# Performance work log

Hardware: AMD Instinct MI355X
Metric: run time of the kernel (lower is better)

The kernel has to match this reference:

```python
import jax, jax.numpy as jnp
import numpy as np

N_NODES = 50000
N_EDGES = 800000
IN_FEATS = 64
K = 4
OUT_FEATS = 256


def setup_inputs() -> dict:
    key = jax.random.key(0)
    k1, k2, k3, k4, k5 = jax.random.split(key, 5)
    signal = jax.random.normal(k1, (N_NODES, IN_FEATS), dtype=jnp.float32)
    src = jax.random.randint(k2, (N_EDGES,), 0, N_NODES, dtype=jnp.int32)
    dst = jax.random.randint(k3, (N_EDGES,), 0, N_NODES, dtype=jnp.int32)
    lambda_max = jnp.array([2.0], dtype=jnp.float32)  # normalized Laplacian bound
    W = jax.random.normal(k4, (IN_FEATS * K, OUT_FEATS), dtype=jnp.float32) * (1.0 / np.sqrt(IN_FEATS * K))
    b = jax.random.normal(k5, (OUT_FEATS,), dtype=jnp.float32) * 0.01
    return {"signal": signal, "src": src, "dst": dst, "lambda_max": lambda_max, "W": W, "b": b}


def reference(signal, src, dst, lambda_max, W, b):
    n = signal.shape[0]
    # in-degrees, clamped to >= 1, then D^{-1/2}
    deg = jax.ops.segment_sum(jnp.ones_like(dst, dtype=signal.dtype), dst, num_segments=n)
    d_sqrt = jnp.power(jnp.clip(deg, 1.0), -0.5)[:, None]  # [N,1]

    def unn_laplacian(x):
        # D^{-1/2} A D^{-1/2} x via gather-from-src, scatter-sum-to-dst
        h = (x * d_sqrt)[src]                                   # [E,f]
        agg = jax.ops.segment_sum(h, dst, num_segments=n)       # [N,f]
        return agg * d_sqrt

    X0 = signal
    Xs = [X0]
    if K > 1:
        re_norm = 2.0 / lambda_max  # broadcasts over nodes ([1] -> [N,f])
        X1 = -re_norm * unn_laplacian(X0) + X0 * (re_norm - 1.0)
        Xs.append(X1)
        for _ in range(2, K):
            Xi = -2.0 * re_norm * unn_laplacian(X1) + X1 * 2.0 * (re_norm - 1.0) - X0
            Xs.append(Xi)
            X1, X0 = Xi, X1
    Xt = jnp.concatenate(Xs, axis=1)  # [N, f*K]
    return jax.nn.relu(Xt @ W + b)
```

## Files before the change

kernel.cpp:

```cpp
#include <hip/hip_runtime.h>

#define NN 50000
#define NE 800000
#define F  64
#define OUTF 256
#define CAP 48
#define NT 3128

#define NPART 8
#define PART_NODES 6250
#define FILL_CHUNKS 256
#define CHUNK_E 3125

typedef __attribute__((ext_vector_type(8))) short    s16x8;
typedef __attribute__((ext_vector_type(8))) _Float16 f16x8;
typedef __attribute__((ext_vector_type(4))) float    f32x4;

static __device__ __forceinline__ unsigned short f2bf(float f) {
    unsigned u = __float_as_uint(f);
    u += 0x7fffu + ((u >> 16) & 1u);
    return (unsigned short)(u >> 16);
}
static __device__ __forceinline__ float bf2f(int h) {
    return __uint_as_float(((unsigned)(h & 0xffff)) << 16);
}
static __device__ __forceinline__ unsigned short f2h(float f) {
    _Float16 h = (_Float16)f;
    return __builtin_bit_cast(unsigned short, h);
}

__global__ __launch_bounds__(256) void fill_kernel(const int* __restrict__ src,
                                                   const int* __restrict__ dst,
                                                   int* __restrict__ cnt,
                                                   int* __restrict__ csr) {
    int part  = blockIdx.x & (NPART - 1);
    int chunk = blockIdx.x >> 3;
    int lo = part * PART_NODES;
    int e0 = chunk * CHUNK_E;
    int e1 = e0 + CHUNK_E;
    for (int e = e0 + threadIdx.x; e < e1; e += 256) {
        int d = dst[e];
        if ((unsigned)(d - lo) < (unsigned)PART_NODES) {
            int s = src[e];
            int k = atomicAdd(&cnt[d], 1);
            if (k < CAP) csr[d * CAP + k] = s;
        }
    }
}


__global__ __launch_bounds__(256) void prep_kernel(const float* __restrict__ sig,
                                                   const int* __restrict__ cnt,
                                                   const float* __restrict__ W,
                                                   unsigned short* __restrict__ XrowH,
                                                   unsigned short* __restrict__ XrowL,
                                                   unsigned short* __restrict__ XfF,
                                                   unsigned short* __restrict__ WfF) {
    int bid = blockIdx.x;
    if (bid < 3125) {
        int i = bid * 256 + threadIdx.x;
        int n = i >> 4, fq = i & 15;
        float d = rsqrtf(fmaxf((float)cnt[n], 1.0f));
        float4 v = *(const float4*)&sig[n * F + fq * 4];
        float yx = v.x * d, yy = v.y * d, yz = v.z * d, yw = v.w * d;
        unsigned short h0 = f2bf(yx), h1 = f2bf(yy), h2 = f2bf(yz), h3 = f2bf(yw);
        unsigned short l0 = f2bf(yx - bf2f(h0)), l1 = f2bf(yy - bf2f(h1));
        unsigned short l2 = f2bf(yz - bf2f(h2)), l3 = f2bf(yw - bf2f(h3));
        *(ushort4*)&XrowH[(size_t)n * 192 + fq * 4] = make_ushort4(h0, h1, h2, h3);
        *(ushort4*)&XrowL[(size_t)n * 192 + fq * 4] = make_ushort4(l0, l1, l2, l3);
        unsigned short u0 = f2h(v.x), u1 = f2h(v.y), u2 = f2h(v.z), u3 = f2h(v.w);
        int t = n >> 4, m = n & 15;
        int k0 = fq >> 3, qq = (fq >> 1) & 3, half = fq & 1;
        size_t base = ((size_t)((t * 8 + k0) * 64 + qq * 16 + m)) * 8 + half * 4;
        *(ushort4*)&XfF[base] = make_ushort4(u0, u1, u2, u3);
    } else {
        int id = (bid - 3125) * 256 + threadIdx.x;
        if (id < 8192) {
            int lane = id & 63, k0 = (id >> 6) & 7, ct = id >> 9;
            int n = lane & 15, q = lane >> 4;
            s16x8 h;
            #pragma unroll
            for (int j = 0; j < 8; ++j) {
                float x = W[(k0 * 32 + q * 8 + j) * OUTF + ct * 16 + n];
                h[j] = (short)f2h(x);
            }
            ((s16x8*)WfF)[id] = h;
        }
    }
}

__global__ __launch_bounds__(256) void lap_kernel(const int* __restrict__ cnt,
                                                  const int* __restrict__ csr,
                                                  const float* __restrict__ lm,
                                                  unsigned short* __restrict__ XrowH,
                                                  unsigned short* __restrict__ XrowL,
                                                  unsigned short* __restrict__ XfF, int p) {
    int lane = threadIdx.x & 63;
    int half = lane >> 5;
    int sub  = lane & 31;
    int q2   = sub >> 4;
    int fq   = sub & 15;
    int wid  = (blockIdx.x * blockDim.x + threadIdx.x) >> 6;
    int n    = wid * 2 + half;
    if (n >= NN) return;
    int dgf = cnt[n];
    int dg  = min(dgf, CAP);
    int cin = p - 1;
    int foff = fq << 2;

    float ax = 0.f, ay = 0.f, az = 0.f, aw = 0.f;
    for (int k = 0; k < dg; k += 16) {
        int   s[8];
        float w[8];
        ushort4 h[8];
        #pragma unroll
        for (int j = 0; j < 8; ++j) {
            int slot = k + q2 + 2 * j;
            int ok   = slot < dg;
            int si   = csr[n * CAP + slot];
            s[j] = ok ? si : 0;
            w[j] = ok ? 1.0f : 0.0f;
        }
        #pragma unroll
        for (int j = 0; j < 8; ++j)
            h[j] = *(const ushort4*)&XrowH[((size_t)s[j] * 3 + cin) * 64 + foff];
        #pragma unroll
        for (int j = 0; j < 8; ++j) {
            ax += bf2f(h[j].x) * w[j];
            ay += bf2f(h[j].y) * w[j];
            az += bf2f(h[j].z) * w[j];
            aw += bf2f(h[j].w) * w[j];
        }
    }
    ax += __shfl_xor(ax, 16);
    ay += __shfl_xor(ay, 16);
    az += __shfl_xor(az, 16);
    aw += __shfl_xor(aw, 16);

    float rn = 2.0f / lm[0];
    float dn = rsqrtf(fmaxf((float)dgf, 1.0f));
    float sq = sqrtf(fmaxf((float)dgf, 1.0f));
    ushort4 xh = *(const ushort4*)&XrowH[((size_t)n * 3 + cin) * 64 + foff];
    ushort4 xl = *(const ushort4*)&XrowL[((size_t)n * 3 + cin) * 64 + foff];
    float x1x = (bf2f(xh.x) + bf2f(xl.x)) * sq;
    float x1y = (bf2f(xh.y) + bf2f(xl.y)) * sq;
    float x1z = (bf2f(xh.z) + bf2f(xl.z)) * sq;
    float x1w = (bf2f(xh.w) + bf2f(xl.w)) * sq;
    float rx, ry, rz, rw;
    if (p == 1) {
        float c1 = rn - 1.0f;
        rx = -rn * dn * ax + x1x * c1;
        ry = -rn * dn * ay + x1y * c1;
        rz = -rn * dn * az + x1z * c1;
        rw = -rn * dn * aw + x1w * c1;
    } else {
        ushort4 zh = *(const ushort4*)&XrowH[((size_t)n * 3 + (p - 2)) * 64 + foff];
        ushort4 zl = *(const ushort4*)&XrowL[((size_t)n * 3 + (p - 2)) * 64 + foff];
        float c1 = 2.0f * (rn - 1.0f);
        rx = -2.0f * rn * dn * ax + x1x * c1 - (bf2f(zh.x) + bf2f(zl.x)) * sq;
        ry = -2.0f * rn * dn * ay + x1y * c1 - (bf2f(zh.y) + bf2f(zl.y)) * sq;
        rz = -2.0f * rn * dn * az + x1z * c1 - (bf2f(zh.z) + bf2f(zl.z)) * sq;
        rw = -2.0f * rn * dn * aw + x1w * c1 - (bf2f(zh.w) + bf2f(zl.w)) * sq;
    }

    float yx = rx * dn, yy = ry * dn, yz = rz * dn, yw = rw * dn;
    unsigned short yh0 = f2bf(yx), yh1 = f2bf(yy), yh2 = f2bf(yz), yh3 = f2bf(yw);
    if (q2 == 0) {
        if (p < 3)
            *(ushort4*)&XrowH[((size_t)n * 3 + p) * 64 + foff] = make_ushort4(yh0, yh1, yh2, yh3);
        unsigned short u0 = f2h(rx), u1 = f2h(ry), u2 = f2h(rz), u3 = f2h(rw);
        int t = n >> 4, m = n & 15;
        int k0 = p * 2 + (fq >> 3), qq = (fq >> 1) & 3, hf = fq & 1;
        size_t fbase = ((size_t)((t * 8 + k0) * 64 + qq * 16 + m)) * 8 + hf * 4;
        *(ushort4*)&XfF[fbase] = make_ushort4(u0, u1, u2, u3);
    } else if (p < 3) {
        unsigned short l0 = f2bf(yx - bf2f(yh0)), l1 = f2bf(yy - bf2f(yh1));
        unsigned short l2 = f2bf(yz - bf2f(yh2)), l3 = f2bf(yw - bf2f(yh3));
        *(ushort4*)&XrowL[((size_t)n * 3 + p) * 64 + foff] = make_ushort4(l0, l1, l2, l3);
    }
}

__global__ __launch_bounds__(512, 2) void gemm_kernel(const unsigned short* __restrict__ XfF,
                                                      const unsigned short* __restrict__ WfF,
                                                      const float* __restrict__ b,
                                                      float* __restrict__ out) {
    int lane = threadIdx.x & 63;
    int w    = threadIdx.x >> 6;
    int rh = w & 1, cg = w >> 1;
    int m = lane & 15, q = lane >> 4;
    int bt0 = blockIdx.x * 8;
    const f16x8* A = (const f16x8*)XfF;
    const f16x8* B = (const f16x8*)WfF;

    f32x4 acc[4][4];
    #pragma unroll
    for (int rt = 0; rt < 4; ++rt)
        #pragma unroll
        for (int c = 0; c < 4; ++c) acc[rt][c] = (f32x4){0.f, 0.f, 0.f, 0.f};

    #pragma unroll
    for (int k0 = 0; k0 < 8; ++k0) {
        f16x8 a[4];
        #pragma unroll
        for (int rt = 0; rt < 4; ++rt)
            a[rt] = A[((bt0 + rh * 4 + rt) * 8 + k0) * 64 + lane];
        #pragma unroll
        for (int c = 0; c < 4; ++c) {
            int ct = cg * 4 + c;
            f16x8 bh = B[(ct * 8 + k0) * 64 + lane];
            #pragma unroll
            for (int rt = 0; rt < 4; ++rt)
                acc[rt][c] = __builtin_amdgcn_mfma_f32_16x16x32_f16(a[rt], bh, acc[rt][c], 0, 0, 0);
        }
    }

    #pragma unroll
    for (int rt = 0; rt < 4; ++rt) {
        int rbase = (bt0 + rh * 4 + rt) * 16 + q * 4;
        #pragma unroll
        for (int c = 0; c < 4; ++c) {
            int col = (cg * 4 + c) * 16 + m;
            float bv = b[col];
            #pragma unroll
            for (int i = 0; i < 4; ++i) {
                int r = rbase + i;
                if (r < NN) out[r * OUTF + col] = fmaxf(acc[rt][c][i] + bv, 0.0f);
            }
        }
    }
}

extern "C" void kernel_launch(void* const* d_in, const int* in_sizes, int n_in,
                              void* d_out, int out_size, void* d_ws, size_t ws_size,
                              hipStream_t stream) {
    const float* signal     = (const float*)d_in[0];
    const int*   src        = (const int*)  d_in[1];
    const int*   dst        = (const int*)  d_in[2];
    const float* lambda_max = (const float*)d_in[3];
    const float* W          = (const float*)d_in[4];
    const float* b          = (const float*)d_in[5];
    float* out = (float*)d_out;

    int*   cnt = (int*)d_ws;
    int*   csr = cnt + NN;
    unsigned short* XrowH = (unsigned short*)(csr + NN * CAP);
    unsigned short* XrowL = XrowH + (size_t)NN * 192;
    unsigned short* XfF   = XrowL + (size_t)NN * 192;
    unsigned short* WfF   = XfF + (size_t)NT * 4096;

    hipMemsetAsync(cnt, 0, NN * sizeof(int), stream);
    fill_kernel<<<NPART * FILL_CHUNKS, 256, 0, stream>>>(src, dst, cnt, csr);
    prep_kernel<<<3125 + 32, 256, 0, stream>>>(signal, cnt, W, XrowH, XrowL, XfF, WfF);

    for (int p = 1; p <= 3; ++p)
        lap_kernel<<<NN / 8, 256, 0, stream>>>(cnt, csr, lambda_max, XrowH, XrowL, XfF, p);

    gemm_kernel<<<391, 512, 0, stream>>>(XfF, WfF, b, out);
}
```

Before: 252.7 us.

## Split prep into separate kernels, precompute inverse sqrt degree, halve GEMM tile

Splits the combined prep kernel into three kernels: one precomputes D^{-1/2} into a buffer, one converts the signal, and one converts W. The Laplacian kernel now reads the precomputed inverse sqrt instead of recomputing it. Separately, the GEMM block tile shrinks from 8 to 4 row tiles per block and the grid doubles to 782 blocks, for more parallelism at lower reuse of W per block. This adds two extra kernel launches and an extra workspace buffer.

```diff
diff --git a/kernel.cpp b/kernel.cpp
--- a/kernel.cpp
+++ b/kernel.cpp
@@ -48,49 +48,53 @@
     }
 }
 
-
-__global__ __launch_bounds__(256) void prep_kernel(const float* __restrict__ sig,
-                                                   const int* __restrict__ cnt,
-                                                   const float* __restrict__ W,
-                                                   unsigned short* __restrict__ XrowH,
-                                                   unsigned short* __restrict__ XrowL,
-                                                   unsigned short* __restrict__ XfF,
-                                                   unsigned short* __restrict__ WfF) {
-    int bid = blockIdx.x;
-    if (bid < 3125) {
-        int i = bid * 256 + threadIdx.x;
-        int n = i >> 4, fq = i & 15;
-        float d = rsqrtf(fmaxf((float)cnt[n], 1.0f));
-        float4 v = *(const float4*)&sig[n * F + fq * 4];
-        float yx = v.x * d, yy = v.y * d, yz = v.z * d, yw = v.w * d;
-        unsigned short h0 = f2bf(yx), h1 = f2bf(yy), h2 = f2bf(yz), h3 = f2bf(yw);
-        unsigned short l0 = f2bf(yx - bf2f(h0)), l1 = f2bf(yy - bf2f(h1));
-        unsigned short l2 = f2bf(yz - bf2f(h2)), l3 = f2bf(yw - bf2f(h3));
-        *(ushort4*)&XrowH[(size_t)n * 192 + fq * 4] = make_ushort4(h0, h1, h2, h3);
-        *(ushort4*)&XrowL[(size_t)n * 192 + fq * 4] = make_ushort4(l0, l1, l2, l3);
-        unsigned short u0 = f2h(v.x), u1 = f2h(v.y), u2 = f2h(v.z), u3 = f2h(v.w);
-        int t = n >> 4, m = n & 15;
-        int k0 = fq >> 3, qq = (fq >> 1) & 3, half = fq & 1;
-        size_t base = ((size_t)((t * 8 + k0) * 64 + qq * 16 + m)) * 8 + half * 4;
-        *(ushort4*)&XfF[base] = make_ushort4(u0, u1, u2, u3);
-    } else {
-        int id = (bid - 3125) * 256 + threadIdx.x;
-        if (id < 8192) {
-            int lane = id & 63, k0 = (id >> 6) & 7, ct = id >> 9;
-            int n = lane & 15, q = lane >> 4;
-            s16x8 h;
-            #pragma unroll
-            for (int j = 0; j < 8; ++j) {
-                float x = W[(k0 * 32 + q * 8 + j) * OUTF + ct * 16 + n];
-                h[j] = (short)f2h(x);
-            }
-            ((s16x8*)WfF)[id] = h;
-        }
-    }
+__global__ void dsqrt_kernel(const int* __restrict__ cnt, float* __restrict__ dsq) {
+    int n = blockIdx.x * blockDim.x + threadIdx.x;
+    if (n < NN) dsq[n] = rsqrtf(fmaxf((float)cnt[n], 1.0f));
+}
+
+
+__global__ void copy0_kernel(const float* __restrict__ sig,
+                             const float* __restrict__ dsq,
+                             unsigned short* __restrict__ XrowH,
+                             unsigned short* __restrict__ XrowL,
+                             unsigned short* __restrict__ XfF) {
+    int i = blockIdx.x * blockDim.x + threadIdx.x;
+    if (i >= NN * 16) return;
+    int n = i >> 4, fq = i & 15;
+    float d = dsq[n];
+    float4 v = *(const float4*)&sig[n * F + fq * 4];
+    float yx = v.x * d, yy = v.y * d, yz = v.z * d, yw = v.w * d;
+    unsigned short h0 = f2bf(yx), h1 = f2bf(yy), h2 = f2bf(yz), h3 = f2bf(yw);
+    unsigned short l0 = f2bf(yx - bf2f(h0)), l1 = f2bf(yy - bf2f(h1));
+    unsigned short l2 = f2bf(yz - bf2f(h2)), l3 = f2bf(yw - bf2f(h3));
+    *(ushort4*)&XrowH[(size_t)n * 192 + fq * 4] = make_ushort4(h0, h1, h2, h3);
+    *(ushort4*)&XrowL[(size_t)n * 192 + fq * 4] = make_ushort4(l0, l1, l2, l3);
+    unsigned short u0 = f2h(v.x), u1 = f2h(v.y), u2 = f2h(v.z), u3 = f2h(v.w);
+    int t = n >> 4, m = n & 15;
+    int k0 = fq >> 3, qq = (fq >> 1) & 3, half = fq & 1;
+    size_t base = ((size_t)((t * 8 + k0) * 64 + qq * 16 + m)) * 8 + half * 4;
+    *(ushort4*)&XfF[base] = make_ushort4(u0, u1, u2, u3);
+}
+
+__global__ void convw_kernel(const float* __restrict__ W,
+                             unsigned short* __restrict__ WfF) {
+    int id = blockIdx.x * blockDim.x + threadIdx.x;
+    if (id >= 8192) return;
+    int lane = id & 63, k0 = (id >> 6) & 7, ct = id >> 9;
+    int n = lane & 15, q = lane >> 4;
+    s16x8 h;
+    #pragma unroll
+    for (int j = 0; j < 8; ++j) {
+        float x = W[(k0 * 32 + q * 8 + j) * OUTF + ct * 16 + n];
+        h[j] = (short)f2h(x);
+    }
+    ((s16x8*)WfF)[id] = h;
 }
 
 __global__ __launch_bounds__(256) void lap_kernel(const int* __restrict__ cnt,
                                                   const int* __restrict__ csr,
+                                                  const float* __restrict__ dsq,
                                                   const float* __restrict__ lm,
                                                   unsigned short* __restrict__ XrowH,
                                                   unsigned short* __restrict__ XrowL,
@@ -138,7 +142,7 @@
     aw += __shfl_xor(aw, 16);
 
     float rn = 2.0f / lm[0];
-    float dn = rsqrtf(fmaxf((float)dgf, 1.0f));
+    float dn = dsq[n];
     float sq = sqrtf(fmaxf((float)dgf, 1.0f));
     ushort4 xh = *(const ushort4*)&XrowH[((size_t)n * 3 + cin) * 64 + foff];
     ushort4 xl = *(const ushort4*)&XrowL[((size_t)n * 3 + cin) * 64 + foff];
@@ -188,35 +192,35 @@
     int w    = threadIdx.x >> 6;
     int rh = w & 1, cg = w >> 1;
     int m = lane & 15, q = lane >> 4;
-    int bt0 = blockIdx.x * 8;
+    int bt0 = blockIdx.x * 4;
     const f16x8* A = (const f16x8*)XfF;
     const f16x8* B = (const f16x8*)WfF;
 
-    f32x4 acc[4][4];
-    #pragma unroll
-    for (int rt = 0; rt < 4; ++rt)
+    f32x4 acc[2][4];
+    #pragma unroll
+    for (int rt = 0; rt < 2; ++rt)
         #pragma unroll
         for (int c = 0; c < 4; ++c) acc[rt][c] = (f32x4){0.f, 0.f, 0.f, 0.f};
 
     #pragma unroll
     for (int k0 = 0; k0 < 8; ++k0) {
-        f16x8 a[4];
-        #pragma unroll
-        for (int rt = 0; rt < 4; ++rt)
-            a[rt] = A[((bt0 + rh * 4 + rt) * 8 + k0) * 64 + lane];
+        f16x8 a[2];
+        #pragma unroll
+        for (int rt = 0; rt < 2; ++rt)
+            a[rt] = A[((bt0 + rh * 2 + rt) * 8 + k0) * 64 + lane];
         #pragma unroll
         for (int c = 0; c < 4; ++c) {
             int ct = cg * 4 + c;
             f16x8 bh = B[(ct * 8 + k0) * 64 + lane];
             #pragma unroll
-            for (int rt = 0; rt < 4; ++rt)
+            for (int rt = 0; rt < 2; ++rt)
                 acc[rt][c] = __builtin_amdgcn_mfma_f32_16x16x32_f16(a[rt], bh, acc[rt][c], 0, 0, 0);
         }
     }
 
     #pragma unroll
-    for (int rt = 0; rt < 4; ++rt) {
-        int rbase = (bt0 + rh * 4 + rt) * 16 + q * 4;
+    for (int rt = 0; rt < 2; ++rt) {
+        int rbase = (bt0 + rh * 2 + rt) * 16 + q * 4;
         #pragma unroll
         for (int c = 0; c < 4; ++c) {
             int col = (cg * 4 + c) * 16 + m;
@@ -243,17 +247,20 @@
 
     int*   cnt = (int*)d_ws;
     int*   csr = cnt + NN;
-    unsigned short* XrowH = (unsigned short*)(csr + NN * CAP);
+    float* dsq = (float*)(csr + (size_t)NN * CAP);
+    unsigned short* XrowH = (unsigned short*)(dsq + NN);
     unsigned short* XrowL = XrowH + (size_t)NN * 192;
     unsigned short* XfF   = XrowL + (size_t)NN * 192;
     unsigned short* WfF   = XfF + (size_t)NT * 4096;
 
     hipMemsetAsync(cnt, 0, NN * sizeof(int), stream);
     fill_kernel<<<NPART * FILL_CHUNKS, 256, 0, stream>>>(src, dst, cnt, csr);
-    prep_kernel<<<3125 + 32, 256, 0, stream>>>(signal, cnt, W, XrowH, XrowL, XfF, WfF);
+    dsqrt_kernel<<<(NN + 255) / 256, 256, 0, stream>>>(cnt, dsq);
+    copy0_kernel<<<(NN * 16 + 255) / 256, 256, 0, stream>>>(signal, dsq, XrowH, XrowL, XfF);
+    convw_kernel<<<32, 256, 0, stream>>>(W, WfF);
 
     for (int p = 1; p <= 3; ++p)
-        lap_kernel<<<NN / 8, 256, 0, stream>>>(cnt, csr, lambda_max, XrowH, XrowL, XfF, p);
-
-    gemm_kernel<<<391, 512, 0, stream>>>(XfF, WfF, b, out);
-}
+        lap_kernel<<<NN / 8, 256, 0, stream>>>(cnt, csr, dsq, lambda_max, XrowH, XrowL, XfF, p);
+
+    gemm_kernel<<<782, 512, 0, stream>>>(XfF, WfF, b, out);
+}
```

Measured after the change: 220.3 us. 1.15x faster.
